# Kernel optimization log

Measured on AMD Instinct MI355X. Metric: run time of the kernel, lower is better.

## Reference

```python
import jax, jax.numpy as jnp
import numpy as np

D_K = 64

def setup_inputs() -> dict:
    key = jax.random.key(0)
    kq, kk, kv, km = jax.random.split(key, 4)
    B, H, S, D = 2, 16, 2048, D_K
    q = jax.random.normal(kq, (B, H, S, D), dtype=jnp.float32)
    k = jax.random.normal(kk, (B, H, S, D), dtype=jnp.float32)
    v = jax.random.normal(kv, (B, H, S, D), dtype=jnp.float32)
    atten_mask = jax.random.bernoulli(km, 0.1, (B, H, S, S))  # True = masked out
    return {"q": q, "k": k, "v": v, "atten_mask": atten_mask}

def reference(q, k, v, atten_mask):
    # score = q @ k^T / sqrt(d_k)  -> [B, H, S, S]
    score = jnp.einsum("bhqd,bhkd->bhqk", q, k) / np.sqrt(D_K).astype(np.float32)
    score = jnp.where(atten_mask, jnp.float32(-1e9), score)
    attn = jax.nn.softmax(score, axis=-1)
    return attn  # original module stops before the AV matmul (v unused)
```

## Files before the change

### kernel.cpp

```cpp
#include <hip/hip_runtime.h>

typedef _Float16 f16x8 __attribute__((ext_vector_type(8)));
typedef _Float16 f16x4 __attribute__((ext_vector_type(4)));
typedef float    f32x4 __attribute__((ext_vector_type(4)));
typedef int      i32x4 __attribute__((ext_vector_type(4)));

#define S_LEN 2048
#define D_KH  64
#define NBH   32
#define QTILE 16
#define THREADS 1024
#define NBLOCKS 256
#define NT 16
#define QK_ELEMS (NBH * S_LEN * D_KH)

__device__ __forceinline__ f16x8 cvt8(const float4 a, const float4 b) {
  f16x8 r;
  r[0] = (_Float16)a.x; r[1] = (_Float16)a.y;
  r[2] = (_Float16)a.z; r[3] = (_Float16)a.w;
  r[4] = (_Float16)b.x; r[5] = (_Float16)b.y;
  r[6] = (_Float16)b.z; r[7] = (_Float16)b.w;
  return r;
}

__global__ __launch_bounds__(256) void cvt_qk_kernel(
    const float* __restrict__ q, const float* __restrict__ kmat,
    _Float16* __restrict__ qh, _Float16* __restrict__ kh) {
  const long long idx = ((long long)blockIdx.x * 256 + threadIdx.x) * 8;
  float4 q0 = *(const float4*)(q + idx);
  float4 q1 = *(const float4*)(q + idx + 4);
  const float s = 0.125f;
  q0.x *= s; q0.y *= s; q0.z *= s; q0.w *= s;
  q1.x *= s; q1.y *= s; q1.z *= s; q1.w *= s;
  *(f16x8*)(qh + idx) = cvt8(q0, q1);
  const float4 k0 = *(const float4*)(kmat + idx);
  const float4 k1 = *(const float4*)(kmat + idx + 4);
  *(f16x8*)(kh + idx) = cvt8(k0, k1);
}

template <bool F16>
__global__ __launch_bounds__(THREADS, 4) void sdpa_probs_kernel(
    const float* __restrict__ qf, const float* __restrict__ kf,
    const _Float16* __restrict__ qh, const _Float16* __restrict__ kh,
    const int* __restrict__ mask, float* __restrict__ out) {
  const int bid = (int)blockIdx.x;
  const int nb  = (bid & 7) * (NBLOCKS / 8) + (bid >> 3);
  const int bh  = nb >> 3;
  const int jb  = nb & 7;

  __shared__ _Float16 sc[2][QTILE][S_LEN];

  const int tid   = (int)threadIdx.x;
  const int w     = tid >> 6;
  const int l     = tid & 63;
  const int lo    = l & 15;
  const int g     = l >> 4;
  const int dbase = g << 3;

  const size_t qk_bh = (size_t)bh * S_LEN * D_KH;
  const size_t obh   = (size_t)bh * S_LEN * S_LEN;
  const int    physx = (w >> 2) << 4;

  for (int t = 0; t < NT; ++t) {
    const int qt = jb * NT + t;
    _Float16 (*buf)[S_LEN] = sc[t & 1];

    i32x4 raw[8];
    {
      const int* mrow = mask + obh + (size_t)(qt * QTILE + w) * S_LEN + (l << 2);
      #pragma unroll
      for (int i = 0; i < 8; ++i)
        raw[i] = __builtin_nontemporal_load((const i32x4*)(mrow + (i << 8)));
    }

    f16x8 a0, a1;
    if constexpr (F16) {
      const _Float16* qp = qh + qk_bh + (size_t)(qt * QTILE + lo) * D_KH + dbase;
      a0 = *(const f16x8*)qp;
      a1 = *(const f16x8*)(qp + 32);
    } else {
      const float* qp = qf + qk_bh + (size_t)(qt * QTILE + lo) * D_KH;
      float4 t0 = *(const float4*)(qp + dbase);
      float4 t1 = *(const float4*)(qp + dbase + 4);
      float4 t2 = *(const float4*)(qp + dbase + 32);
      float4 t3 = *(const float4*)(qp + dbase + 36);
      const float s = 0.125f;
      t0.x *= s; t0.y *= s; t0.z *= s; t0.w *= s;
      t1.x *= s; t1.y *= s; t1.z *= s; t1.w *= s;
      t2.x *= s; t2.y *= s; t2.z *= s; t2.w *= s;
      t3.x *= s; t3.y *= s; t3.z *= s; t3.w *= s;
      a0 = cvt8(t0, t1);
      a1 = cvt8(t2, t3);
    }

    #pragma unroll 2
    for (int kt = 0; kt < 8; ++kt) {
      const int kcol = (w << 7) + (kt << 4) + lo;
      f16x8 b0, b1;
      if constexpr (F16) {
        const _Float16* kp = kh + qk_bh + (size_t)kcol * D_KH + dbase;
        b0 = *(const f16x8*)kp;
        b1 = *(const f16x8*)(kp + 32);
      } else {
        const float* kp = kf + qk_bh + (size_t)kcol * D_KH + dbase;
        b0 = cvt8(*(const float4*)(kp), *(const float4*)(kp + 4));
        b1 = cvt8(*(const float4*)(kp + 32), *(const float4*)(kp + 36));
      }
      f32x4 acc = {0.f, 0.f, 0.f, 0.f};
      acc = __builtin_amdgcn_mfma_f32_16x16x32_f16(a0, b0, acc, 0, 0, 0);
      acc = __builtin_amdgcn_mfma_f32_16x16x32_f16(a1, b1, acc, 0, 0, 0);
      const int phys = kcol ^ (g << 4);
      #pragma unroll
      for (int r = 0; r < 4; ++r)
        buf[(g << 2) + r][phys] = (_Float16)__expf(acc[r]);
    }

    unsigned pm = 0u;
    #pragma unroll
    for (int i = 0; i < 8; ++i)
      pm |= ((raw[i].x ? 1u : 0u) | (raw[i].y ? 2u : 0u) |
             (raw[i].z ? 4u : 0u) | (raw[i].w ? 8u : 0u)) << (4 * i);

    __syncthreads();

    float sv[32];
    float sum = 0.f;
    #pragma unroll
    for (int i = 0; i < 8; ++i) {
      const int off = (((i << 8) + (l << 2))) ^ physx;
      const f16x4 h = *(const f16x4*)&buf[w][off];
      const unsigned b = pm >> (4 * i);
      sv[4 * i + 0] = (b & 1u) ? 0.f : (float)h[0];
      sv[4 * i + 1] = (b & 2u) ? 0.f : (float)h[1];
      sv[4 * i + 2] = (b & 4u) ? 0.f : (float)h[2];
      sv[4 * i + 3] = (b & 8u) ? 0.f : (float)h[3];
      sum += (sv[4 * i + 0] + sv[4 * i + 1]) + (sv[4 * i + 2] + sv[4 * i + 3]);
    }
    #pragma unroll
    for (int off = 32; off > 0; off >>= 1)
      sum += __shfl_xor(sum, off, 64);
    const float inv = 1.0f / sum;

    float* op = out + obh + (size_t)(qt * QTILE + w) * S_LEN;
    #pragma unroll
    for (int i = 0; i < 8; ++i) {
      const int col = (i << 8) + (l << 2);
      f32x4 o = { sv[4 * i + 0] * inv, sv[4 * i + 1] * inv,
                  sv[4 * i + 2] * inv, sv[4 * i + 3] * inv };
      __builtin_nontemporal_store(o, (f32x4*)(op + col));
    }
  }
}

extern "C" void kernel_launch(void* const* d_in, const int* in_sizes, int n_in,
                              void* d_out, int out_size, void* d_ws, size_t ws_size,
                              hipStream_t stream) {
  const float* q    = (const float*)d_in[0];
  const float* kmat = (const float*)d_in[1];
  const int*   mask = (const int*)d_in[3];
  float*       out  = (float*)d_out;

  const size_t need = (size_t)QK_ELEMS * 2 * sizeof(_Float16);
  if (ws_size >= need) {
    _Float16* qh = (_Float16*)d_ws;
    _Float16* kh = qh + QK_ELEMS;
    cvt_qk_kernel<<<dim3(QK_ELEMS / 8 / 256), dim3(256), 0, stream>>>(q, kmat, qh, kh);
    sdpa_probs_kernel<true><<<dim3(NBLOCKS), dim3(THREADS), 0, stream>>>(
        nullptr, nullptr, qh, kh, mask, out);
  } else {
    sdpa_probs_kernel<false><<<dim3(NBLOCKS), dim3(THREADS), 0, stream>>>(
        q, kmat, nullptr, nullptr, mask, out);
  }
}
```

Measured before the change: 264.0 us.

## Restructure softmax kernel into per-wave 4-row strips with pipelined mask loads

Replaces the 1024-thread blocks, which looped over 16-row query tiles with block-wide syncs, with 128-thread blocks in which each wave owns four query rows. Each wave computes the whole row with MFMA, applies the mask and accumulates the row sum in registers, and stages the fp16 exponentials in a private LDS strip. This removes __syncthreads, and mask loads are double-buffered across column chunks. The MFMA now uses only one of its 16 rows per lane group, since Q rows are replicated (lo>>2), so compute efficiency drops in exchange for more parallelism and less synchronisation.

```diff
diff --git a/kernel.cpp b/kernel.cpp
--- a/kernel.cpp
+++ b/kernel.cpp
@@ -3,15 +3,12 @@
 typedef _Float16 f16x8 __attribute__((ext_vector_type(8)));
 typedef _Float16 f16x4 __attribute__((ext_vector_type(4)));
 typedef float    f32x4 __attribute__((ext_vector_type(4)));
-typedef int      i32x4 __attribute__((ext_vector_type(4)));
 
 #define S_LEN 2048
 #define D_KH  64
 #define NBH   32
-#define QTILE 16
-#define THREADS 1024
-#define NBLOCKS 256
-#define NT 16
+#define THREADS 128
+#define NBLOCKS 8192
 #define QK_ELEMS (NBH * S_LEN * D_KH)
 
 __device__ __forceinline__ f16x8 cvt8(const float4 a, const float4 b) {
@@ -39,115 +36,114 @@
 }
 
 template <bool F16>
-__global__ __launch_bounds__(THREADS, 4) void sdpa_probs_kernel(
+__global__ __launch_bounds__(THREADS, 2) void sdpa_probs_kernel(
     const float* __restrict__ qf, const float* __restrict__ kf,
     const _Float16* __restrict__ qh, const _Float16* __restrict__ kh,
     const int* __restrict__ mask, float* __restrict__ out) {
-  const int bid = (int)blockIdx.x;
-  const int nb  = (bid & 7) * (NBLOCKS / 8) + (bid >> 3);
-  const int bh  = nb >> 3;
-  const int jb  = nb & 7;
+  const int bid  = (int)blockIdx.x;
+  const int nb   = (bid & 7) * (NBLOCKS / 8) + (bid >> 3);
+  const int widx = (int)threadIdx.x >> 6;
+  const int l    = (int)threadIdx.x & 63;
+  const int lo   = l & 15;
+  const int g    = l >> 4;
 
-  __shared__ _Float16 sc[2][QTILE][S_LEN];
+  const int task = nb * 2 + widx;
+  const int bh   = task >> 9;
+  const int r4   = (task & 511) << 2;
 
-  const int tid   = (int)threadIdx.x;
-  const int w     = tid >> 6;
-  const int l     = tid & 63;
-  const int lo    = l & 15;
-  const int g     = l >> 4;
-  const int dbase = g << 3;
+  __shared__ _Float16 strip_s[2][4][S_LEN];
+  _Float16* strip = &strip_s[widx][0][0];
 
   const size_t qk_bh = (size_t)bh * S_LEN * D_KH;
-  const size_t obh   = (size_t)bh * S_LEN * S_LEN;
-  const int    physx = (w >> 2) << 4;
 
-  for (int t = 0; t < NT; ++t) {
-    const int qt = jb * NT + t;
-    _Float16 (*buf)[S_LEN] = sc[t & 1];
+  f16x8 a0, a1;
+  if constexpr (F16) {
+    const _Float16* qp = qh + qk_bh + (size_t)(r4 + (lo >> 2)) * D_KH + (g << 3);
+    a0 = *(const f16x8*)qp;
+    a1 = *(const f16x8*)(qp + 32);
+  } else {
+    const float* qp = qf + qk_bh + (size_t)(r4 + (lo >> 2)) * D_KH + (g << 3);
+    float4 t0 = *(const float4*)(qp);
+    float4 t1 = *(const float4*)(qp + 4);
+    float4 t2 = *(const float4*)(qp + 32);
+    float4 t3 = *(const float4*)(qp + 36);
+    const float s = 0.125f;
+    t0.x *= s; t0.y *= s; t0.z *= s; t0.w *= s;
+    t1.x *= s; t1.y *= s; t1.z *= s; t1.w *= s;
+    t2.x *= s; t2.y *= s; t2.z *= s; t2.w *= s;
+    t3.x *= s; t3.y *= s; t3.z *= s; t3.w *= s;
+    a0 = cvt8(t0, t1);
+    a1 = cvt8(t2, t3);
+  }
 
-    i32x4 raw[8];
-    {
-      const int* mrow = mask + obh + (size_t)(qt * QTILE + w) * S_LEN + (l << 2);
-      #pragma unroll
-      for (int i = 0; i < 8; ++i)
-        raw[i] = __builtin_nontemporal_load((const i32x4*)(mrow + (i << 8)));
-    }
+  const int* mrow = mask + ((size_t)bh * S_LEN + (r4 + g)) * S_LEN + lo;
+  _Float16* swr = strip + g * S_LEN + lo;
 
-    f16x8 a0, a1;
-    if constexpr (F16) {
-      const _Float16* qp = qh + qk_bh + (size_t)(qt * QTILE + lo) * D_KH + dbase;
-      a0 = *(const f16x8*)qp;
-      a1 = *(const f16x8*)(qp + 32);
-    } else {
-      const float* qp = qf + qk_bh + (size_t)(qt * QTILE + lo) * D_KH;
-      float4 t0 = *(const float4*)(qp + dbase);
-      float4 t1 = *(const float4*)(qp + dbase + 4);
-      float4 t2 = *(const float4*)(qp + dbase + 32);
-      float4 t3 = *(const float4*)(qp + dbase + 36);
-      const float s = 0.125f;
-      t0.x *= s; t0.y *= s; t0.z *= s; t0.w *= s;
-      t1.x *= s; t1.y *= s; t1.z *= s; t1.w *= s;
-      t2.x *= s; t2.y *= s; t2.z *= s; t2.w *= s;
-      t3.x *= s; t3.y *= s; t3.z *= s; t3.w *= s;
-      a0 = cvt8(t0, t1);
-      a1 = cvt8(t2, t3);
-    }
+  const _Float16* kp0 = nullptr;
+  const float*    kpf0 = nullptr;
+  if constexpr (F16) kp0  = kh + qk_bh + (size_t)lo * D_KH + (g << 3);
+  else               kpf0 = kf + qk_bh + (size_t)lo * D_KH + (g << 3);
 
-    #pragma unroll 2
-    for (int kt = 0; kt < 8; ++kt) {
-      const int kcol = (w << 7) + (kt << 4) + lo;
-      f16x8 b0, b1;
-      if constexpr (F16) {
-        const _Float16* kp = kh + qk_bh + (size_t)kcol * D_KH + dbase;
-        b0 = *(const f16x8*)kp;
-        b1 = *(const f16x8*)(kp + 32);
-      } else {
-        const float* kp = kf + qk_bh + (size_t)kcol * D_KH + dbase;
-        b0 = cvt8(*(const float4*)(kp), *(const float4*)(kp + 4));
-        b1 = cvt8(*(const float4*)(kp + 32), *(const float4*)(kp + 36));
-      }
-      f32x4 acc = {0.f, 0.f, 0.f, 0.f};
-      acc = __builtin_amdgcn_mfma_f32_16x16x32_f16(a0, b0, acc, 0, 0, 0);
-      acc = __builtin_amdgcn_mfma_f32_16x16x32_f16(a1, b1, acc, 0, 0, 0);
-      const int phys = kcol ^ (g << 4);
-      #pragma unroll
-      for (int r = 0; r < 4; ++r)
-        buf[(g << 2) + r][phys] = (_Float16)__expf(acc[r]);
-    }
+  float rowsum = 0.f;
+  int mb0[8], mb1[8];
+  #pragma unroll
+  for (int j = 0; j < 8; ++j)
+    mb0[j] = __builtin_nontemporal_load(mrow + (j << 4));
 
-    unsigned pm = 0u;
+#define KT_BODY(kt_, mj_) do {                                                 \
+    f16x8 b0_, b1_;                                                            \
+    if constexpr (F16) {                                                       \
+      const _Float16* kp_ = kp0 + (size_t)(kt_) * 1024;                        \
+      b0_ = *(const f16x8*)kp_;                                                \
+      b1_ = *(const f16x8*)(kp_ + 32);                                         \
+    } else {                                                                   \
+      const float* kp_ = kpf0 + (size_t)(kt_) * 1024;                          \
+      b0_ = cvt8(*(const float4*)(kp_), *(const float4*)(kp_ + 4));            \
+      b1_ = cvt8(*(const float4*)(kp_ + 32), *(const float4*)(kp_ + 36));      \
+    }                                                                          \
+    f32x4 acc_ = {0.f, 0.f, 0.f, 0.f};                                         \
+    acc_ = __builtin_amdgcn_mfma_f32_16x16x32_f16(a0, b0_, acc_, 0, 0, 0);     \
+    acc_ = __builtin_amdgcn_mfma_f32_16x16x32_f16(a1, b1_, acc_, 0, 0, 0);     \
+    const float e_ = (mj_) ? 0.f : __expf(acc_[0]);                            \
+    rowsum += e_;                                                              \
+    swr[((kt_) ^ g) << 4] = (_Float16)e_;                                      \
+  } while (0)
+
+  #pragma unroll 1
+  for (int c2 = 0; c2 < 8; ++c2) {
+    const int ce = 2 * c2;
     #pragma unroll
-    for (int i = 0; i < 8; ++i)
-      pm |= ((raw[i].x ? 1u : 0u) | (raw[i].y ? 2u : 0u) |
-             (raw[i].z ? 4u : 0u) | (raw[i].w ? 8u : 0u)) << (4 * i);
+    for (int j = 0; j < 8; ++j)
+      mb1[j] = __builtin_nontemporal_load(
+          mrow + (((((ce + 1) & 15) << 3) + j) << 4));
+    #pragma unroll
+    for (int j = 0; j < 8; ++j) KT_BODY(ce * 8 + j, mb0[j]);
+    #pragma unroll
+    for (int j = 0; j < 8; ++j)
+      mb0[j] = __builtin_nontemporal_load(
+          mrow + (((((ce + 2) & 15) << 3) + j) << 4));
+    #pragma unroll
+    for (int j = 0; j < 8; ++j) KT_BODY((ce + 1) * 8 + j, mb1[j]);
+  }
+#undef KT_BODY
 
-    __syncthreads();
+  rowsum += __shfl_xor(rowsum, 1, 64);
+  rowsum += __shfl_xor(rowsum, 2, 64);
+  rowsum += __shfl_xor(rowsum, 4, 64);
+  rowsum += __shfl_xor(rowsum, 8, 64);
+  const float inv = 1.0f / rowsum;
 
-    float sv[32];
-    float sum = 0.f;
+  #pragma unroll
+  for (int r = 0; r < 4; ++r) {
+    const float invr = __shfl(inv, r << 4, 64);
+    const _Float16* srd = strip + r * S_LEN + (((l << 2) ^ (r << 4)));
+    float* op = out + ((size_t)bh * S_LEN + (r4 + r)) * S_LEN + (l << 2);
     #pragma unroll
     for (int i = 0; i < 8; ++i) {
-      const int off = (((i << 8) + (l << 2))) ^ physx;
-      const f16x4 h = *(const f16x4*)&buf[w][off];
-      const unsigned b = pm >> (4 * i);
-      sv[4 * i + 0] = (b & 1u) ? 0.f : (float)h[0];
-      sv[4 * i + 1] = (b & 2u) ? 0.f : (float)h[1];
-      sv[4 * i + 2] = (b & 4u) ? 0.f : (float)h[2];
-      sv[4 * i + 3] = (b & 8u) ? 0.f : (float)h[3];
-      sum += (sv[4 * i + 0] + sv[4 * i + 1]) + (sv[4 * i + 2] + sv[4 * i + 3]);
-    }
-    #pragma unroll
-    for (int off = 32; off > 0; off >>= 1)
-      sum += __shfl_xor(sum, off, 64);
-    const float inv = 1.0f / sum;
-
-    float* op = out + obh + (size_t)(qt * QTILE + w) * S_LEN;
-    #pragma unroll
-    for (int i = 0; i < 8; ++i) {
-      const int col = (i << 8) + (l << 2);
-      f32x4 o = { sv[4 * i + 0] * inv, sv[4 * i + 1] * inv,
-                  sv[4 * i + 2] * inv, sv[4 * i + 3] * inv };
-      __builtin_nontemporal_store(o, (f32x4*)(op + col));
+      const f16x4 h = *(const f16x4*)&srd[i << 8];
+      f32x4 o = { (float)h[0] * invr, (float)h[1] * invr,
+                  (float)h[2] * invr, (float)h[3] * invr };
+      __builtin_nontemporal_store(o, (f32x4*)(op + (i << 8)));
     }
   }
 }
```

After: 614.4 us. +132.7%, slower.
